# Performance work log

Measured on AMD Instinct MI355X. Metric: run time of the kernel, lower is better.

## Reference

```python
import jax, jax.numpy as jnp
import numpy as np
from jax import lax

EPS = 1e-5

def _groupnorm1(v, scale, bias):
    # GroupNorm(1, C) on [bs, C] vectors (spatial dims are 1x1): normalize over C per sample
    m = jnp.mean(v, axis=-1, keepdims=True)
    var = jnp.mean((v - m) ** 2, axis=-1, keepdims=True)
    return (v - m) / jnp.sqrt(var + EPS) * scale + bias

def _mish(v):
    return v * jnp.tanh(jax.nn.softplus(v))


def setup_inputs() -> dict:
    key = jax.random.key(0)
    ks = jax.random.split(key, 5)
    bs, C, H, W = 32, 128, 64, 64
    K, red = 4, 16
    hid = C // red
    return {
        "x": jax.random.normal(ks[0], (bs, C, H, W), jnp.float32),
        "weight": jax.random.normal(ks[1], (K, C, C, 3, 3), jnp.float32) * 0.05,
        "bias": jax.random.normal(ks[2], (K, C), jnp.float32) * 0.05,
        "se_w1": jax.random.normal(ks[3], (hid, C), jnp.float32) * 0.1,
        "gn1_scale": jnp.ones((hid,), jnp.float32),
        "gn1_bias": jnp.zeros((hid,), jnp.float32),
        "se_w2": jax.random.normal(ks[4], (K, hid), jnp.float32) * 0.1,
        "gn2_scale": jnp.ones((K,), jnp.float32),
        "gn2_bias": jnp.zeros((K,), jnp.float32),
    }


def reference(x, weight, bias, se_w1, gn1_scale, gn1_bias, se_w2, gn2_scale, gn2_bias):
    bs, C, H, W = x.shape
    K, out_p, in_p, kh, kw = weight.shape

    # --- SqueezeAndExcitation attention -> [bs, K] in (0,1) ---
    pooled = jnp.mean(x, axis=(2, 3))                       # [bs, C]
    h1 = pooled @ se_w1.T                                   # [bs, hid] (1x1 conv, no bias)
    h1 = _mish(_groupnorm1(h1, gn1_scale, gn1_bias))
    h2 = h1 @ se_w2.T                                       # [bs, K]
    att = jax.nn.sigmoid(_groupnorm1(h2, gn2_scale, gn2_bias))

    # --- per-sample kernel / bias aggregation ---
    agg_w = jnp.einsum('bk,koihw->boihw', att, weight)      # [bs, out, in, kh, kw]
    agg_b = att @ bias                                      # [bs, out]

    # --- per-sample conv2d (equivalent to groups=bs grouped conv in torch) ---
    pad = ((1, 1), (1, 1))
    def per_sample(xi, wi):
        return lax.conv_general_dilated(
            xi[None], wi, window_strides=(1, 1), padding=pad,
            dimension_numbers=('NCHW', 'OIHW', 'NCHW'))[0]
    out = jax.vmap(per_sample)(x, agg_w)                    # [bs, out, H, W]
    return out + agg_b[:, :, None, None]
```

## Files before the change

### kernel.cpp

```cpp
#include <hip/hip_runtime.h>
#include <hip/hip_bf16.h>
#include <math.h>
#include <stdint.h>

#define EPS 1e-5f

typedef __attribute__((ext_vector_type(8))) short bf16x8;
typedef __attribute__((ext_vector_type(16))) float f32x16;

__device__ __forceinline__ ushort f2bf(float f) {
    union { float f; unsigned u; } v; v.f = f;
    unsigned r = (v.u + 0x7FFFu + ((v.u >> 16) & 1u)) >> 16;
    return (ushort)r;
}

__device__ __forceinline__ void dma16(const void* g, void* l) {
    __builtin_amdgcn_global_load_lds(
        (__attribute__((address_space(1))) const void*)(uintptr_t)g,
        (__attribute__((address_space(3))) void*)(uintptr_t)l,
        16, 0, 0);
}

__global__ __launch_bounds__(256) void transpose_kernel(const float* __restrict__ x,
                                                        ushort* __restrict__ xT,
                                                        float* __restrict__ pooled) {
    __shared__ float T2[64][132];
    int bid = blockIdx.x;
    int b = (bid & 7) * 4 + (bid >> 9);
    int y = (bid >> 3) & 63;
    int t = threadIdx.x;

    int ic2 = t >> 1, half = t & 1;
    const float4* src = (const float4*)(x + (((size_t)b * 128 + ic2) * 64 + y) * 64 + half * 32);
    float s = 0.f;
#pragma unroll
    for (int i = 0; i < 8; ++i) {
        float4 v = src[i];
        int c0 = half * 32 + i * 4;
        T2[c0][ic2] = v.x; T2[c0 + 1][ic2] = v.y; T2[c0 + 2][ic2] = v.z; T2[c0 + 3][ic2] = v.w;
        s += v.x + v.y + v.z + v.w;
    }
    s += __shfl_xor(s, 1, 64);
    if (half == 0) atomicAdd(&pooled[b * 128 + ic2], s * (1.0f / 4096.0f));
    __syncthreads();

    int col = t >> 2, icq = t & 3;
    const float4* row = (const float4*)&T2[col][icq * 32];
    uint pk[16];
#pragma unroll
    for (int m = 0; m < 8; ++m) {
        float4 v = row[m];
        pk[2 * m]     = (uint)f2bf(v.x) | ((uint)f2bf(v.y) << 16);
        pk[2 * m + 1] = (uint)f2bf(v.z) | ((uint)f2bf(v.w) << 16);
    }
    ushort* dst = xT + (((size_t)(b * 66 + y + 1)) * 66 + col + 1) * 128 + icq * 32;
    ((uint4*)dst)[0] = make_uint4(pk[0], pk[1], pk[2], pk[3]);
    ((uint4*)dst)[1] = make_uint4(pk[4], pk[5], pk[6], pk[7]);
    ((uint4*)dst)[2] = make_uint4(pk[8], pk[9], pk[10], pk[11]);
    ((uint4*)dst)[3] = make_uint4(pk[12], pk[13], pk[14], pk[15]);

    uint4 z = make_uint4(0, 0, 0, 0);
    if (y == 0) {
        uint4* row0 = (uint4*)(xT + ((size_t)b * 66 + 0) * 66 * 128);
        for (int i = t; i < 1056; i += 256) row0[i] = z;
    }
    if (y == 63) {
        uint4* row65 = (uint4*)(xT + ((size_t)b * 66 + 65) * 66 * 128);
        for (int i = t; i < 1056; i += 256) row65[i] = z;
    }
    if (t < 32) {
        int c = (t >> 4) * 65;
        int i = t & 15;
        *(uint4*)(xT + (((size_t)(b * 66 + y + 1)) * 66 + c) * 128 + i * 8) = z;
    }
}

__global__ __launch_bounds__(256) void aggw_kernel(const float* __restrict__ weight,
                                                   const float* __restrict__ pooled,
                                                   const float* __restrict__ se_w1,
                                                   const float* __restrict__ gn1_s, const float* __restrict__ gn1_b,
                                                   const float* __restrict__ se_w2,
                                                   const float* __restrict__ gn2_s, const float* __restrict__ gn2_b,
                                                   float* __restrict__ att_out,
                                                   ushort* __restrict__ aggw) {
    __shared__ float pl[8][128];
    __shared__ float h1s[8][8];
    __shared__ float att_s[8][4];
    int blk = blockIdx.x;
    int rep = blk / 72;
    int t = threadIdx.x;

#pragma unroll
    for (int u = 0; u < 4; ++u) {
        int pid = u * 256 + t;
        int bl = pid >> 7, ic = pid & 127;
        pl[bl][ic] = pooled[(rep * 8 + bl) * 128 + ic];
    }
    __syncthreads();
    if (t < 64) {
        int bl = t >> 3, jj = t & 7;
        float s1 = 0.f;
        for (int c = 0; c < 128; ++c) s1 += pl[bl][c] * se_w1[jj * 128 + c];
        h1s[bl][jj] = s1;
    }
    __syncthreads();
    if (t < 8) {
        float h1[8];
#pragma unroll
        for (int j = 0; j < 8; ++j) h1[j] = h1s[t][j];
        float m = 0.f;
#pragma unroll
        for (int j = 0; j < 8; ++j) m += h1[j];
        m *= 0.125f;
        float var = 0.f;
#pragma unroll
        for (int j = 0; j < 8; ++j) { float d = h1[j] - m; var += d * d; }
        var *= 0.125f;
        float inv = rsqrtf(var + EPS);
#pragma unroll
        for (int j = 0; j < 8; ++j) {
            float tt = (h1[j] - m) * inv * gn1_s[j] + gn1_b[j];
            float sp = (tt > 20.f) ? tt : log1pf(expf(tt));
            h1[j] = tt * tanhf(sp);
        }
        float h2[4];
#pragma unroll
        for (int k = 0; k < 4; ++k) {
            float s2 = 0.f;
#pragma unroll
            for (int j = 0; j < 8; ++j) s2 += h1[j] * se_w2[k * 8 + j];
            h2[k] = s2;
        }
        float m2 = 0.25f * (h2[0] + h2[1] + h2[2] + h2[3]);
        float v2 = 0.f;
#pragma unroll
        for (int k = 0; k < 4; ++k) { float d = h2[k] - m2; v2 += d * d; }
        v2 *= 0.25f;
        float inv2 = rsqrtf(v2 + EPS);
#pragma unroll
        for (int k = 0; k < 4; ++k) {
            float tt = (h2[k] - m2) * inv2 * gn2_s[k] + gn2_b[k];
            att_s[t][k] = 1.0f / (1.0f + expf(-tt));
        }
    }
    __syncthreads();

    if ((blk % 72) == 0 && t < 32) att_out[rep * 32 + t] = att_s[t >> 2][t & 3];

    int tq = (blk % 72) * 256 + t;
    int tap = tq >> 10;
    int within = tq & 1023;
    int oc = within >> 3;
    int p = within & 7;
    int g = (p - oc) & 7;
    int h = tap / 9, s = tap % 9;
    int ic0 = h * 64 + g * 8;

    float wv[4][8];
#pragma unroll
    for (int k = 0; k < 4; ++k)
#pragma unroll
        for (int j = 0; j < 8; ++j)
            wv[k][j] = weight[(((size_t)(k * 128 + oc)) * 128 + ic0 + j) * 9 + s];

#pragma unroll
    for (int bl = 0; bl < 8; ++bl) {
        int b = rep * 8 + bl;
        float a0 = att_s[bl][0], a1 = att_s[bl][1], a2 = att_s[bl][2], a3 = att_s[bl][3];
        uint pk[4];
#pragma unroll
        for (int q = 0; q < 4; ++q) {
            float f0 = a0 * wv[0][2 * q] + a1 * wv[1][2 * q] + a2 * wv[2][2 * q] + a3 * wv[3][2 * q];
            float f1 = a0 * wv[0][2 * q + 1] + a1 * wv[1][2 * q + 1] + a2 * wv[2][2 * q + 1] + a3 * wv[3][2 * q + 1];
            pk[q] = (uint)f2bf(f0) | ((uint)f2bf(f1) << 16);
        }
        *(uint4*)(aggw + (size_t)b * 147456 + (size_t)tq * 8) = make_uint4(pk[0], pk[1], pk[2], pk[3]);
    }
}

__global__ __launch_bounds__(512, 2) void conv_kernel(const ushort* __restrict__ xT,
                                                      const ushort* __restrict__ aggw,
                                                      const float* __restrict__ att,
                                                      const float* __restrict__ bias,
                                                      float* __restrict__ out) {
    __shared__ ushort ldsB[660 * 64];

    int bid = blockIdx.x;
    int xcd = bid & 7;
    int j = bid >> 3;
    int b = xcd * 4 + (j >> 3);
    int tile = j & 7;
    int y0 = tile * 8;

    int tid = threadIdx.x;
    int l = tid & 63, w = tid >> 6;
    int wm = w >> 2, wn = w & 3;
    int l31 = l & 31, lhi = l >> 5;

    const ushort* xTb = xT + ((size_t)(b * 66 + y0)) * 66 * 128;
    const ushort* Asmp = aggw + (size_t)b * 147456;

    int ocofs[2], rotA[2];
#pragma unroll
    for (int mi = 0; mi < 2; ++mi) {
        int oc = wm * 64 + mi * 32 + l31;
        ocofs[mi] = oc * 64;
        rotA[mi] = (lhi + oc) & 7;
    }
    int CB[4];
#pragma unroll
    for (int nb = 0; nb < 4; ++nb)
        CB[nb] = (2 * wn + (nb >> 1)) * 66 + (nb & 1) * 32 + l31;
    int rotB = (l31 + lhi) & 7;

    f32x16 acc[2][4];
#pragma unroll
    for (int mi = 0; mi < 2; ++mi)
#pragma unroll
        for (int nb = 0; nb < 4; ++nb)
#pragma unroll
            for (int q = 0; q < 16; ++q) acc[mi][nb][q] = 0.f;

    bf16x8 a[2][4];
#pragma unroll
    for (int mi = 0; mi < 2; ++mi)
#pragma unroll
        for (int icb = 0; icb < 4; ++icb)
            a[mi][icb] = *(const bf16x8*)(Asmp + ocofs[mi] + (((rotA[mi] + 2 * icb) & 7) << 3));

#pragma unroll
    for (int i = 0; i < 11; ++i) {
        int k = i * 512 + tid;
        if (k < 5280) {
            int rc = k >> 3;
            int c = rc % 66;
            int g = ((k & 7) - c) & 7;
            dma16(xTb + (size_t)rc * 128 + (g << 3), &ldsB[(size_t)k * 8]);
        }
    }
    __syncthreads();

    for (int hs = 0; hs < 18; ++hs) {
        int s = (hs >= 9) ? hs - 9 : hs;
        int kh = s / 3, kw = s - kh * 3;
        int celladd = kh * 66 + kw;
        const ushort* Anext = Asmp + (size_t)(hs + 1) * 8192;
#pragma unroll
        for (int icb = 0; icb < 4; ++icb) {
            int slotb = (rotB + 2 * icb + kw) & 7;
            bf16x8 bb[4];
#pragma unroll
            for (int nb = 0; nb < 4; ++nb) {
                int cell = CB[nb] + celladd;
                bb[nb] = *(const bf16x8*)&ldsB[(cell << 6) + (slotb << 3)];
            }
#pragma unroll
            for (int mi = 0; mi < 2; ++mi)
#pragma unroll
                for (int nb = 0; nb < 4; ++nb)
                    acc[mi][nb] = __builtin_amdgcn_mfma_f32_32x32x16_bf16(a[mi][icb], bb[nb], acc[mi][nb], 0, 0, 0);
            if (hs < 17) {
#pragma unroll
                for (int mi = 0; mi < 2; ++mi)
                    a[mi][icb] = *(const bf16x8*)(Anext + ocofs[mi] + (((rotA[mi] + 2 * icb) & 7) << 3));
            }
        }
        if (hs == 8) {
            __syncthreads();
#pragma unroll
            for (int i = 0; i < 11; ++i) {
                int k = i * 512 + tid;
                if (k < 5280) {
                    int rc = k >> 3;
                    int c = rc % 66;
                    int g = ((k & 7) - c) & 7;
                    dma16(xTb + (size_t)rc * 128 + 64 + (g << 3), &ldsB[(size_t)k * 8]);
                }
            }
            __syncthreads();
        }
    }

    float a0 = att[b * 4 + 0], a1 = att[b * 4 + 1], a2 = att[b * 4 + 2], a3 = att[b * 4 + 3];
#pragma unroll
    for (int mi = 0; mi < 2; ++mi)
#pragma unroll
        for (int q = 0; q < 16; ++q) {
            int oc = wm * 64 + mi * 32 + (q & 3) + 8 * (q >> 2) + 4 * lhi;
            float ab = a0 * bias[oc] + a1 * bias[128 + oc] + a2 * bias[256 + oc] + a3 * bias[384 + oc];
#pragma unroll
            for (int nb = 0; nb < 4; ++nb) {
                int y = y0 + 2 * wn + (nb >> 1);
                out[(((size_t)b * 128 + oc) * 64 + y) * 64 + (nb & 1) * 32 + l31] = acc[mi][nb][q] + ab;
            }
        }
}

extern "C" void kernel_launch(void* const* d_in, const int* in_sizes, int n_in,
                              void* d_out, int out_size, void* d_ws, size_t ws_size,
                              hipStream_t stream) {
    const float* x      = (const float*)d_in[0];
    const float* weight = (const float*)d_in[1];
    const float* bias   = (const float*)d_in[2];
    const float* se_w1  = (const float*)d_in[3];
    const float* gn1_s  = (const float*)d_in[4];
    const float* gn1_b  = (const float*)d_in[5];
    const float* se_w2  = (const float*)d_in[6];
    const float* gn2_s  = (const float*)d_in[7];
    const float* gn2_b  = (const float*)d_in[8];
    float* out = (float*)d_out;

    float*  att    = (float*)d_ws;
    float*  pooled = (float*)((char*)d_ws + 16384);
    ushort* aggw   = (ushort*)((char*)d_ws + 65536);
    ushort* xT     = (ushort*)((char*)d_ws + 10485760);

    hipMemsetAsync(pooled, 0, 128 * 32 * sizeof(float), stream);
    transpose_kernel<<<2048, 256, 0, stream>>>(x, xT, pooled);
    aggw_kernel<<<288, 256, 0, stream>>>(weight, pooled, se_w1, gn1_s, gn1_b,
                                         se_w2, gn2_s, gn2_b, att, aggw);
    conv_kernel<<<256, 512, 0, stream>>>(xT, aggw, att, bias, out);
}
```

Measured before the change: 92.69 us.

## Restructure conv tiles to reuse B fragments across kernel rows, reorder aggw taps

The conv kernel moves to 256-thread blocks, each covering 4 output rows, and launches 512 blocks. For each kw and input-channel block it loads B fragments for 4 input rows once and reuses them across all three kh taps, with A fragments double-buffered in registers. The aggregated-weight layout is permuted to kw-major tap order to match this loop. The transpose kernel also changes its LDS layout so the writes are row-wise float4 stores and the reads are strided column loads. The aim is fewer LDS reads per MFMA and smaller LDS staging, at the cost of more register pressure and larger halo overhead, since the halo is 6 staged rows per 4 output rows.

```diff
diff --git a/kernel.cpp b/kernel.cpp
--- a/kernel.cpp
+++ b/kernel.cpp
@@ -24,7 +24,7 @@
 __global__ __launch_bounds__(256) void transpose_kernel(const float* __restrict__ x,
                                                         ushort* __restrict__ xT,
                                                         float* __restrict__ pooled) {
-    __shared__ float T2[64][132];
+    __shared__ float T[128][68];
     int bid = blockIdx.x;
     int b = (bid & 7) * 4 + (bid >> 9);
     int y = (bid >> 3) & 63;
@@ -32,26 +32,25 @@
 
     int ic2 = t >> 1, half = t & 1;
     const float4* src = (const float4*)(x + (((size_t)b * 128 + ic2) * 64 + y) * 64 + half * 32);
+    float4* trow = (float4*)&T[ic2][half * 32];
     float s = 0.f;
 #pragma unroll
     for (int i = 0; i < 8; ++i) {
         float4 v = src[i];
-        int c0 = half * 32 + i * 4;
-        T2[c0][ic2] = v.x; T2[c0 + 1][ic2] = v.y; T2[c0 + 2][ic2] = v.z; T2[c0 + 3][ic2] = v.w;
+        trow[i] = v;
         s += v.x + v.y + v.z + v.w;
     }
     s += __shfl_xor(s, 1, 64);
     if (half == 0) atomicAdd(&pooled[b * 128 + ic2], s * (1.0f / 4096.0f));
     __syncthreads();
 
-    int col = t >> 2, icq = t & 3;
-    const float4* row = (const float4*)&T2[col][icq * 32];
+    int col = t & 63, icq = t >> 6;
     uint pk[16];
 #pragma unroll
-    for (int m = 0; m < 8; ++m) {
-        float4 v = row[m];
-        pk[2 * m]     = (uint)f2bf(v.x) | ((uint)f2bf(v.y) << 16);
-        pk[2 * m + 1] = (uint)f2bf(v.z) | ((uint)f2bf(v.w) << 16);
+    for (int jj = 0; jj < 16; ++jj) {
+        float f0 = T[icq * 32 + 2 * jj][col];
+        float f1 = T[icq * 32 + 2 * jj + 1][col];
+        pk[jj] = (uint)f2bf(f0) | ((uint)f2bf(f1) << 16);
     }
     ushort* dst = xT + (((size_t)(b * 66 + y + 1)) * 66 + col + 1) * 128 + icq * 32;
     ((uint4*)dst)[0] = make_uint4(pk[0], pk[1], pk[2], pk[3]);
@@ -153,7 +152,8 @@
     int oc = within >> 3;
     int p = within & 7;
     int g = (p - oc) & 7;
-    int h = tap / 9, s = tap % 9;
+    int h = tap / 9, sp_ = tap % 9;
+    int ws = (sp_ % 3) * 3 + sp_ / 3;
     int ic0 = h * 64 + g * 8;
 
     float wv[4][8];
@@ -161,7 +161,7 @@
     for (int k = 0; k < 4; ++k)
 #pragma unroll
         for (int j = 0; j < 8; ++j)
-            wv[k][j] = weight[(((size_t)(k * 128 + oc)) * 128 + ic0 + j) * 9 + s];
+            wv[k][j] = weight[(((size_t)(k * 128 + oc)) * 128 + ic0 + j) * 9 + ws];
 
 #pragma unroll
     for (int bl = 0; bl < 8; ++bl) {
@@ -178,23 +178,23 @@
     }
 }
 
-__global__ __launch_bounds__(512, 2) void conv_kernel(const ushort* __restrict__ xT,
+__global__ __launch_bounds__(256, 2) void conv_kernel(const ushort* __restrict__ xT,
                                                       const ushort* __restrict__ aggw,
                                                       const float* __restrict__ att,
                                                       const float* __restrict__ bias,
                                                       float* __restrict__ out) {
-    __shared__ ushort ldsB[660 * 64];
+    __shared__ ushort ldsB[396 * 64];
 
     int bid = blockIdx.x;
     int xcd = bid & 7;
-    int j = bid >> 3;
-    int b = xcd * 4 + (j >> 3);
-    int tile = j & 7;
-    int y0 = tile * 8;
+    int idx = bid >> 3;
+    int b = xcd * 4 + (idx >> 4);
+    int tile = idx & 15;
+    int y0 = tile * 4;
 
     int tid = threadIdx.x;
     int l = tid & 63, w = tid >> 6;
-    int wm = w >> 2, wn = w & 3;
+    int wm = w >> 1, wn = w & 1;
     int l31 = l & 31, lhi = l >> 5;
 
     const ushort* xTb = xT + ((size_t)(b * 66 + y0)) * 66 * 128;
@@ -207,11 +207,6 @@
         ocofs[mi] = oc * 64;
         rotA[mi] = (lhi + oc) & 7;
     }
-    int CB[4];
-#pragma unroll
-    for (int nb = 0; nb < 4; ++nb)
-        CB[nb] = (2 * wn + (nb >> 1)) * 66 + (nb & 1) * 32 + l31;
-    int rotB = (l31 + lhi) & 7;
 
     f32x16 acc[2][4];
 #pragma unroll
@@ -221,63 +216,89 @@
 #pragma unroll
             for (int q = 0; q < 16; ++q) acc[mi][nb][q] = 0.f;
 
-    bf16x8 a[2][4];
-#pragma unroll
-    for (int mi = 0; mi < 2; ++mi)
-#pragma unroll
-        for (int icb = 0; icb < 4; ++icb)
-            a[mi][icb] = *(const bf16x8*)(Asmp + ocofs[mi] + (((rotA[mi] + 2 * icb) & 7) << 3));
-
-#pragma unroll
-    for (int i = 0; i < 11; ++i) {
-        int k = i * 512 + tid;
-        if (k < 5280) {
-            int rc = k >> 3;
-            int c = rc % 66;
-            int g = ((k & 7) - c) & 7;
-            dma16(xTb + (size_t)rc * 128 + (g << 3), &ldsB[(size_t)k * 8]);
-        }
-    }
-    __syncthreads();
-
-    for (int hs = 0; hs < 18; ++hs) {
-        int s = (hs >= 9) ? hs - 9 : hs;
-        int kh = s / 3, kw = s - kh * 3;
-        int celladd = kh * 66 + kw;
-        const ushort* Anext = Asmp + (size_t)(hs + 1) * 8192;
+    bf16x8 aR[2][3][2];
+
+#define LOADA(P, H, KW, ICB)                                                                 \
+    {                                                                                        \
+        const ushort* tb_ = Asmp + (size_t)((H) * 9 + (KW) * 3) * 8192;                      \
+        _Pragma("unroll")                                                                    \
+        for (int kh_ = 0; kh_ < 3; ++kh_)                                                    \
+            _Pragma("unroll")                                                                \
+            for (int mi_ = 0; mi_ < 2; ++mi_)                                                \
+                aR[P][kh_][mi_] = *(const bf16x8*)(tb_ + kh_ * 8192 + ocofs[mi_] +           \
+                    (((rotA[mi_] + 2 * (ICB)) & 7) << 3));                                   \
+    }
+
+#define STAGE(H)                                                                             \
+    {                                                                                        \
+        _Pragma("unroll")                                                                    \
+        for (int i_ = 0; i_ < 13; ++i_) {                                                    \
+            int k_ = i_ * 256 + tid;                                                         \
+            if (k_ < 3168) {                                                                 \
+                int rc_ = k_ >> 3;                                                           \
+                int c_ = rc_ % 66;                                                           \
+                int g_ = ((k_ & 7) - c_) & 7;                                                \
+                dma16(xTb + (size_t)rc_ * 128 + (H) * 64 + (g_ << 3),                        \
+                      &ldsB[(size_t)k_ * 8]);                                                \
+            }                                                                                \
+        }                                                                                    \
+    }
+
+#define GROUP(CUR, KW, ICB)                                                                  \
+    {                                                                                        \
+        int c0_ = l31 + (KW);                                                                \
+        int c1_ = 32 + l31 + (KW);                                                           \
+        int s0_ = (2 * (ICB) + lhi + c0_) & 7;                                               \
+        int s1_ = (2 * (ICB) + lhi + c1_) & 7;                                               \
+        bf16x8 B_[4][2];                                                                     \
+        _Pragma("unroll")                                                                    \
+        for (int rr_ = 0; rr_ < 4; ++rr_) {                                                  \
+            int cell0_ = (2 * wn + rr_) * 66 + c0_;                                          \
+            int cell1_ = (2 * wn + rr_) * 66 + c1_;                                          \
+            B_[rr_][0] = *(const bf16x8*)&ldsB[(cell0_ << 6) + (s0_ << 3)];                  \
+            B_[rr_][1] = *(const bf16x8*)&ldsB[(cell1_ << 6) + (s1_ << 3)];                  \
+        }                                                                                    \
+        _Pragma("unroll")                                                                    \
+        for (int kh_ = 0; kh_ < 3; ++kh_)                                                    \
+            _Pragma("unroll")                                                                \
+            for (int mi_ = 0; mi_ < 2; ++mi_)                                                \
+                _Pragma("unroll")                                                            \
+                for (int rp_ = 0; rp_ < 2; ++rp_)                                            \
+                    _Pragma("unroll")                                                        \
+                    for (int ch_ = 0; ch_ < 2; ++ch_)                                        \
+                        acc[mi_][rp_ * 2 + ch_] = __builtin_amdgcn_mfma_f32_32x32x16_bf16(   \
+                            aR[CUR][kh_][mi_], B_[kh_ + rp_][ch_], acc[mi_][rp_ * 2 + ch_],  \
+                            0, 0, 0);                                                        \
+    }
+
+    STAGE(0);
+    LOADA(0, 0, 0, 0);
+    __syncthreads();
+
+#pragma unroll
+    for (int kw = 0; kw < 3; ++kw) {
 #pragma unroll
         for (int icb = 0; icb < 4; ++icb) {
-            int slotb = (rotB + 2 * icb + kw) & 7;
-            bf16x8 bb[4];
-#pragma unroll
-            for (int nb = 0; nb < 4; ++nb) {
-                int cell = CB[nb] + celladd;
-                bb[nb] = *(const bf16x8*)&ldsB[(cell << 6) + (slotb << 3)];
-            }
-#pragma unroll
-            for (int mi = 0; mi < 2; ++mi)
-#pragma unroll
-                for (int nb = 0; nb < 4; ++nb)
-                    acc[mi][nb] = __builtin_amdgcn_mfma_f32_32x32x16_bf16(a[mi][icb], bb[nb], acc[mi][nb], 0, 0, 0);
-            if (hs < 17) {
-#pragma unroll
-                for (int mi = 0; mi < 2; ++mi)
-                    a[mi][icb] = *(const bf16x8*)(Anext + ocofs[mi] + (((rotA[mi] + 2 * icb) & 7) << 3));
-            }
-        }
-        if (hs == 8) {
-            __syncthreads();
-#pragma unroll
-            for (int i = 0; i < 11; ++i) {
-                int k = i * 512 + tid;
-                if (k < 5280) {
-                    int rc = k >> 3;
-                    int c = rc % 66;
-                    int g = ((k & 7) - c) & 7;
-                    dma16(xTb + (size_t)rc * 128 + 64 + (g << 3), &ldsB[(size_t)k * 8]);
-                }
-            }
-            __syncthreads();
+            const int cur = icb & 1;
+            if (icb < 3)      { LOADA(cur ^ 1, 0, kw, icb + 1); }
+            else if (kw < 2)  { LOADA(cur ^ 1, 0, kw + 1, 0); }
+            else              { LOADA(cur ^ 1, 1, 0, 0); }
+            GROUP(cur, kw, icb);
+        }
+    }
+
+    __syncthreads();
+    STAGE(1);
+    __syncthreads();
+
+#pragma unroll
+    for (int kw = 0; kw < 3; ++kw) {
+#pragma unroll
+        for (int icb = 0; icb < 4; ++icb) {
+            const int cur = icb & 1;
+            if (icb < 3)      { LOADA(cur ^ 1, 1, kw, icb + 1); }
+            else if (kw < 2)  { LOADA(cur ^ 1, 1, kw + 1, 0); }
+            GROUP(cur, kw, icb);
         }
     }
 
@@ -294,6 +315,9 @@
                 out[(((size_t)b * 128 + oc) * 64 + y) * 64 + (nb & 1) * 32 + l31] = acc[mi][nb][q] + ab;
             }
         }
+#undef LOADA
+#undef STAGE
+#undef GROUP
 }
 
 extern "C" void kernel_launch(void* const* d_in, const int* in_sizes, int n_in,
@@ -319,5 +343,5 @@
     transpose_kernel<<<2048, 256, 0, stream>>>(x, xT, pooled);
     aggw_kernel<<<288, 256, 0, stream>>>(weight, pooled, se_w1, gn1_s, gn1_b,
                                          se_w2, gn2_s, gn2_b, att, aggw);
-    conv_kernel<<<256, 512, 0, stream>>>(xT, aggw, att, bias, out);
-}
+    conv_kernel<<<512, 256, 0, stream>>>(xT, aggw, att, bias, out);
+}
```

Result: slower. 98.35 us (+6.1%).

## Retile conv to 4-row tiles with 4-wave blocks and change transpose LDS layout

Applied to the files above, without the earlier changes.

The conv kernel now covers 4 output rows per block with 256 threads, and each wave owns one output row across all 128 output channels (4x2 MFMA tiles). The grid doubles to 512 blocks, with a smaller LDS halo buffer. This raises block count and per-wave A-fragment reuse, but means more halo reloading and more A loads from global per MFMA. Separately, the transpose kernel stores rows contiguously into LDS as float4 and does the strided reads on the column side instead.

```diff
diff --git a/kernel.cpp b/kernel.cpp
--- a/kernel.cpp
+++ b/kernel.cpp
@@ -24,7 +24,7 @@
 __global__ __launch_bounds__(256) void transpose_kernel(const float* __restrict__ x,
                                                         ushort* __restrict__ xT,
                                                         float* __restrict__ pooled) {
-    __shared__ float T2[64][132];
+    __shared__ float T[128][68];
     int bid = blockIdx.x;
     int b = (bid & 7) * 4 + (bid >> 9);
     int y = (bid >> 3) & 63;
@@ -32,26 +32,25 @@
 
     int ic2 = t >> 1, half = t & 1;
     const float4* src = (const float4*)(x + (((size_t)b * 128 + ic2) * 64 + y) * 64 + half * 32);
+    float4* trow = (float4*)&T[ic2][half * 32];
     float s = 0.f;
 #pragma unroll
     for (int i = 0; i < 8; ++i) {
         float4 v = src[i];
-        int c0 = half * 32 + i * 4;
-        T2[c0][ic2] = v.x; T2[c0 + 1][ic2] = v.y; T2[c0 + 2][ic2] = v.z; T2[c0 + 3][ic2] = v.w;
+        trow[i] = v;
         s += v.x + v.y + v.z + v.w;
     }
     s += __shfl_xor(s, 1, 64);
     if (half == 0) atomicAdd(&pooled[b * 128 + ic2], s * (1.0f / 4096.0f));
     __syncthreads();
 
-    int col = t >> 2, icq = t & 3;
-    const float4* row = (const float4*)&T2[col][icq * 32];
+    int col = t & 63, icq = t >> 6;
     uint pk[16];
 #pragma unroll
-    for (int m = 0; m < 8; ++m) {
-        float4 v = row[m];
-        pk[2 * m]     = (uint)f2bf(v.x) | ((uint)f2bf(v.y) << 16);
-        pk[2 * m + 1] = (uint)f2bf(v.z) | ((uint)f2bf(v.w) << 16);
+    for (int jj = 0; jj < 16; ++jj) {
+        float f0 = T[icq * 32 + 2 * jj][col];
+        float f1 = T[icq * 32 + 2 * jj + 1][col];
+        pk[jj] = (uint)f2bf(f0) | ((uint)f2bf(f1) << 16);
     }
     ushort* dst = xT + (((size_t)(b * 66 + y + 1)) * 66 + col + 1) * 128 + icq * 32;
     ((uint4*)dst)[0] = make_uint4(pk[0], pk[1], pk[2], pk[3]);
@@ -178,60 +177,58 @@
     }
 }
 
-__global__ __launch_bounds__(512, 2) void conv_kernel(const ushort* __restrict__ xT,
+__global__ __launch_bounds__(256, 2) void conv_kernel(const ushort* __restrict__ xT,
                                                       const ushort* __restrict__ aggw,
                                                       const float* __restrict__ att,
                                                       const float* __restrict__ bias,
                                                       float* __restrict__ out) {
-    __shared__ ushort ldsB[660 * 64];
+    __shared__ ushort ldsB[396 * 64];
 
     int bid = blockIdx.x;
     int xcd = bid & 7;
-    int j = bid >> 3;
-    int b = xcd * 4 + (j >> 3);
-    int tile = j & 7;
-    int y0 = tile * 8;
+    int idx = bid >> 3;
+    int b = xcd * 4 + (idx >> 4);
+    int tile = idx & 15;
+    int y0 = tile * 4;
 
     int tid = threadIdx.x;
-    int l = tid & 63, w = tid >> 6;
-    int wm = w >> 2, wn = w & 3;
+    int l = tid & 63, wn = tid >> 6;
     int l31 = l & 31, lhi = l >> 5;
 
     const ushort* xTb = xT + ((size_t)(b * 66 + y0)) * 66 * 128;
     const ushort* Asmp = aggw + (size_t)b * 147456;
 
-    int ocofs[2], rotA[2];
-#pragma unroll
-    for (int mi = 0; mi < 2; ++mi) {
-        int oc = wm * 64 + mi * 32 + l31;
+    int ocofs[4], rotA[4];
+#pragma unroll
+    for (int mi = 0; mi < 4; ++mi) {
+        int oc = mi * 32 + l31;
         ocofs[mi] = oc * 64;
         rotA[mi] = (lhi + oc) & 7;
     }
-    int CB[4];
-#pragma unroll
-    for (int nb = 0; nb < 4; ++nb)
-        CB[nb] = (2 * wn + (nb >> 1)) * 66 + (nb & 1) * 32 + l31;
+    int CB[2];
+#pragma unroll
+    for (int ch = 0; ch < 2; ++ch) CB[ch] = wn * 66 + ch * 32 + l31;
     int rotB = (l31 + lhi) & 7;
 
-    f32x16 acc[2][4];
-#pragma unroll
-    for (int mi = 0; mi < 2; ++mi)
-#pragma unroll
-        for (int nb = 0; nb < 4; ++nb)
-#pragma unroll
-            for (int q = 0; q < 16; ++q) acc[mi][nb][q] = 0.f;
-
-    bf16x8 a[2][4];
-#pragma unroll
-    for (int mi = 0; mi < 2; ++mi)
+    f32x16 acc[4][2];
+#pragma unroll
+    for (int mi = 0; mi < 4; ++mi)
+#pragma unroll
+        for (int ch = 0; ch < 2; ++ch)
+#pragma unroll
+            for (int q = 0; q < 16; ++q) acc[mi][ch][q] = 0.f;
+
+    bf16x8 a[4][4];
+#pragma unroll
+    for (int mi = 0; mi < 4; ++mi)
 #pragma unroll
         for (int icb = 0; icb < 4; ++icb)
             a[mi][icb] = *(const bf16x8*)(Asmp + ocofs[mi] + (((rotA[mi] + 2 * icb) & 7) << 3));
 
 #pragma unroll
-    for (int i = 0; i < 11; ++i) {
-        int k = i * 512 + tid;
-        if (k < 5280) {
+    for (int i = 0; i < 13; ++i) {
+        int k = i * 256 + tid;
+        if (k < 3168) {
             int rc = k >> 3;
             int c = rc % 66;
             int g = ((k & 7) - c) & 7;
@@ -248,29 +245,29 @@
 #pragma unroll
         for (int icb = 0; icb < 4; ++icb) {
             int slotb = (rotB + 2 * icb + kw) & 7;
-            bf16x8 bb[4];
-#pragma unroll
-            for (int nb = 0; nb < 4; ++nb) {
-                int cell = CB[nb] + celladd;
-                bb[nb] = *(const bf16x8*)&ldsB[(cell << 6) + (slotb << 3)];
+            bf16x8 bb[2];
+#pragma unroll
+            for (int ch = 0; ch < 2; ++ch) {
+                int cell = CB[ch] + celladd;
+                bb[ch] = *(const bf16x8*)&ldsB[(cell << 6) + (slotb << 3)];
             }
 #pragma unroll
-            for (int mi = 0; mi < 2; ++mi)
-#pragma unroll
-                for (int nb = 0; nb < 4; ++nb)
-                    acc[mi][nb] = __builtin_amdgcn_mfma_f32_32x32x16_bf16(a[mi][icb], bb[nb], acc[mi][nb], 0, 0, 0);
+            for (int mi = 0; mi < 4; ++mi)
+#pragma unroll
+                for (int ch = 0; ch < 2; ++ch)
+                    acc[mi][ch] = __builtin_amdgcn_mfma_f32_32x32x16_bf16(a[mi][icb], bb[ch], acc[mi][ch], 0, 0, 0);
             if (hs < 17) {
 #pragma unroll
-                for (int mi = 0; mi < 2; ++mi)
+                for (int mi = 0; mi < 4; ++mi)
                     a[mi][icb] = *(const bf16x8*)(Anext + ocofs[mi] + (((rotA[mi] + 2 * icb) & 7) << 3));
             }
         }
         if (hs == 8) {
             __syncthreads();
 #pragma unroll
-            for (int i = 0; i < 11; ++i) {
-                int k = i * 512 + tid;
-                if (k < 5280) {
+            for (int i = 0; i < 13; ++i) {
+                int k = i * 256 + tid;
+                if (k < 3168) {
                     int rc = k >> 3;
                     int c = rc % 66;
                     int g = ((k & 7) - c) & 7;
@@ -282,17 +279,16 @@
     }
 
     float a0 = att[b * 4 + 0], a1 = att[b * 4 + 1], a2 = att[b * 4 + 2], a3 = att[b * 4 + 3];
-#pragma unroll
-    for (int mi = 0; mi < 2; ++mi)
+    int y = y0 + wn;
+#pragma unroll
+    for (int mi = 0; mi < 4; ++mi)
 #pragma unroll
         for (int q = 0; q < 16; ++q) {
-            int oc = wm * 64 + mi * 32 + (q & 3) + 8 * (q >> 2) + 4 * lhi;
+            int oc = mi * 32 + (q & 3) + 8 * (q >> 2) + 4 * lhi;
             float ab = a0 * bias[oc] + a1 * bias[128 + oc] + a2 * bias[256 + oc] + a3 * bias[384 + oc];
 #pragma unroll
-            for (int nb = 0; nb < 4; ++nb) {
-                int y = y0 + 2 * wn + (nb >> 1);
-                out[(((size_t)b * 128 + oc) * 64 + y) * 64 + (nb & 1) * 32 + l31] = acc[mi][nb][q] + ab;
-            }
+            for (int ch = 0; ch < 2; ++ch)
+                out[(((size_t)b * 128 + oc) * 64 + y) * 64 + ch * 32 + l31] = acc[mi][ch][q] + ab;
         }
 }
 
@@ -319,5 +315,5 @@
     transpose_kernel<<<2048, 256, 0, stream>>>(x, xT, pooled);
     aggw_kernel<<<288, 256, 0, stream>>>(weight, pooled, se_w1, gn1_s, gn1_b,
                                          se_w2, gn2_s, gn2_b, att, aggw);
-    conv_kernel<<<256, 512, 0, stream>>>(xT, aggw, att, bias, out);
-}
+    conv_kernel<<<512, 256, 0, stream>>>(xT, aggw, att, bias, out);
+}
```

After: 98.90 us. 1.07x slower.

## Halve conv tile to 4 rows with 256-thread blocks and restructure transpose LDS layout

Applied to the files above, without the earlier changes.

The conv kernel now processes 4 output rows per block with 4 waves instead of 8 rows with 8 waves, doubling the grid to 512 blocks and shrinking the LDS input tile. This aims at better occupancy and load balance across CUs, at the cost of more redundant halo loads and less reuse of the aggregated weights per block. The transpose kernel now stores rows with float4 writes to a [C][W] padded LDS array and transposes on read instead of on write. The epilogue indexing is not visible and may need to match the new tile mapping.

```diff
diff --git a/kernel.cpp b/kernel.cpp
--- a/kernel.cpp
+++ b/kernel.cpp
@@ -24,7 +24,7 @@
 __global__ __launch_bounds__(256) void transpose_kernel(const float* __restrict__ x,
                                                         ushort* __restrict__ xT,
                                                         float* __restrict__ pooled) {
-    __shared__ float T2[64][132];
+    __shared__ float T[128][68];
     int bid = blockIdx.x;
     int b = (bid & 7) * 4 + (bid >> 9);
     int y = (bid >> 3) & 63;
@@ -32,12 +32,12 @@
 
     int ic2 = t >> 1, half = t & 1;
     const float4* src = (const float4*)(x + (((size_t)b * 128 + ic2) * 64 + y) * 64 + half * 32);
+    float4* trow = (float4*)&T[ic2][half * 32];
     float s = 0.f;
 #pragma unroll
     for (int i = 0; i < 8; ++i) {
         float4 v = src[i];
-        int c0 = half * 32 + i * 4;
-        T2[c0][ic2] = v.x; T2[c0 + 1][ic2] = v.y; T2[c0 + 2][ic2] = v.z; T2[c0 + 3][ic2] = v.w;
+        trow[i] = v;
         s += v.x + v.y + v.z + v.w;
     }
     s += __shfl_xor(s, 1, 64);
@@ -45,13 +45,12 @@
     __syncthreads();
 
     int col = t >> 2, icq = t & 3;
-    const float4* row = (const float4*)&T2[col][icq * 32];
     uint pk[16];
 #pragma unroll
-    for (int m = 0; m < 8; ++m) {
-        float4 v = row[m];
-        pk[2 * m]     = (uint)f2bf(v.x) | ((uint)f2bf(v.y) << 16);
-        pk[2 * m + 1] = (uint)f2bf(v.z) | ((uint)f2bf(v.w) << 16);
+    for (int jj = 0; jj < 16; ++jj) {
+        float f0 = T[icq * 32 + 2 * jj][col];
+        float f1 = T[icq * 32 + 2 * jj + 1][col];
+        pk[jj] = (uint)f2bf(f0) | ((uint)f2bf(f1) << 16);
     }
     ushort* dst = xT + (((size_t)(b * 66 + y + 1)) * 66 + col + 1) * 128 + icq * 32;
     ((uint4*)dst)[0] = make_uint4(pk[0], pk[1], pk[2], pk[3]);
@@ -178,39 +177,42 @@
     }
 }
 
-__global__ __launch_bounds__(512, 2) void conv_kernel(const ushort* __restrict__ xT,
+__global__ __launch_bounds__(256, 2) void conv_kernel(const ushort* __restrict__ xT,
                                                       const ushort* __restrict__ aggw,
                                                       const float* __restrict__ att,
                                                       const float* __restrict__ bias,
                                                       float* __restrict__ out) {
-    __shared__ ushort ldsB[660 * 64];
+    __shared__ ushort ldsB[396 * 64];
 
     int bid = blockIdx.x;
     int xcd = bid & 7;
-    int j = bid >> 3;
-    int b = xcd * 4 + (j >> 3);
-    int tile = j & 7;
-    int y0 = tile * 8;
+    int idx = bid >> 3;
+    int b = xcd * 4 + (idx >> 4);
+    int tile = idx & 15;
+    int y0 = tile * 4;
 
     int tid = threadIdx.x;
     int l = tid & 63, w = tid >> 6;
-    int wm = w >> 2, wn = w & 3;
+    int wm = w >> 1, wn = w & 1;
     int l31 = l & 31, lhi = l >> 5;
 
     const ushort* xTb = xT + ((size_t)(b * 66 + y0)) * 66 * 128;
     const ushort* Asmp = aggw + (size_t)b * 147456;
 
-    int ocofs[2], rotA[2];
+    const ushort* ptrA[2];
+    int rotA[2];
 #pragma unroll
     for (int mi = 0; mi < 2; ++mi) {
         int oc = wm * 64 + mi * 32 + l31;
-        ocofs[mi] = oc * 64;
+        ptrA[mi] = Asmp + oc * 64;
         rotA[mi] = (lhi + oc) & 7;
     }
     int CB[4];
 #pragma unroll
-    for (int nb = 0; nb < 4; ++nb)
-        CB[nb] = (2 * wn + (nb >> 1)) * 66 + (nb & 1) * 32 + l31;
+    for (int nb = 0; nb < 4; ++nb) {
+        int rs = nb >> 1, ch = nb & 1;
+        CB[nb] = (2 * wn + rs) * 66 + ch * 32 + l31;
+    }
     int rotB = (l31 + lhi) & 7;
 
     f32x16 acc[2][4];
@@ -226,12 +228,12 @@
     for (int mi = 0; mi < 2; ++mi)
 #pragma unroll
         for (int icb = 0; icb < 4; ++icb)
-            a[mi][icb] = *(const bf16x8*)(Asmp + ocofs[mi] + (((rotA[mi] + 2 * icb) & 7) << 3));
-
-#pragma unroll
-    for (int i = 0; i < 11; ++i) {
-        int k = i * 512 + tid;
-        if (k < 5280) {
+            a[mi][icb] = *(const bf16x8*)(ptrA[mi] + (((rotA[mi] + 2 * icb) & 7) << 3));
+
+#pragma unroll
+    for (int i = 0; i < 13; ++i) {
+        int k = i * 256 + tid;
+        if (k < 3168) {
             int rc = k >> 3;
             int c = rc % 66;
             int g = ((k & 7) - c) & 7;
@@ -261,16 +263,18 @@
                     acc[mi][nb] = __builtin_amdgcn_mfma_f32_32x32x16_bf16(a[mi][icb], bb[nb], acc[mi][nb], 0, 0, 0);
             if (hs < 17) {
 #pragma unroll
-                for (int mi = 0; mi < 2; ++mi)
-                    a[mi][icb] = *(const bf16x8*)(Anext + ocofs[mi] + (((rotA[mi] + 2 * icb) & 7) << 3));
+                for (int mi = 0; mi < 2; ++mi) {
+                    int oc64 = (wm * 64 + mi * 32 + l31) * 64;
+                    a[mi][icb] = *(const bf16x8*)(Anext + oc64 + (((rotA[mi] + 2 * icb) & 7) << 3));
+                }
             }
         }
         if (hs == 8) {
             __syncthreads();
 #pragma unroll
-            for (int i = 0; i < 11; ++i) {
-                int k = i * 512 + tid;
-                if (k < 5280) {
+            for (int i = 0; i < 13; ++i) {
+                int k = i * 256 + tid;
+                if (k < 3168) {
                     int rc = k >> 3;
                     int c = rc % 66;
                     int g = ((k & 7) - c) & 7;
@@ -319,5 +323,5 @@
     transpose_kernel<<<2048, 256, 0, stream>>>(x, xT, pooled);
     aggw_kernel<<<288, 256, 0, stream>>>(weight, pooled, se_w1, gn1_s, gn1_b,
                                          se_w2, gn2_s, gn2_b, att, aggw);
-    conv_kernel<<<256, 512, 0, stream>>>(xT, aggw, att, bias, out);
-}
+    conv_kernel<<<512, 256, 0, stream>>>(xT, aggw, att, bias, out);
+}
```

After: 91.36 us. No clear change (-1.4%).
